# Kernel tuning notes

Hardware: AMD Instinct MI355X
Metric: run time of the kernel (lower is better)

The kernel has to match this reference:

```python
import jax, jax.numpy as jnp
import numpy as np

B, S, D, H, FF = 8, 1024, 2048, 16, 8192
Dh = D // H
EPS = 1e-5

def _layernorm(x, g, b):
    m = jnp.mean(x, axis=-1, keepdims=True)
    v = jnp.mean(jnp.square(x - m), axis=-1, keepdims=True)
    return (x - m) / jnp.sqrt(v + EPS) * g + b

def setup_inputs() -> dict:
    key = jax.random.key(0)
    ks = jax.random.split(key, 12)
    sc_d = 1.0 / np.sqrt(D)
    sc_ff = 1.0 / np.sqrt(FF)
    return {
        "x": jax.random.normal(ks[0], (B, S, D), dtype=jnp.float32),
        "mask": jnp.ones((S, S), dtype=jnp.int32),
        "Wq": jax.random.normal(ks[1], (D, D), dtype=jnp.float32) * sc_d,
        "bq": jnp.zeros((D,), dtype=jnp.float32),
        "Wk": jax.random.normal(ks[2], (D, D), dtype=jnp.float32) * sc_d,
        "bk": jnp.zeros((D,), dtype=jnp.float32),
        "Wv": jax.random.normal(ks[3], (D, D), dtype=jnp.float32) * sc_d,
        "bv": jnp.zeros((D,), dtype=jnp.float32),
        "Wo": jax.random.normal(ks[4], (D, D), dtype=jnp.float32) * sc_d,
        "bo": jnp.zeros((D,), dtype=jnp.float32),
        "W1": jax.random.normal(ks[5], (FF, D), dtype=jnp.float32) * sc_d,
        "b1": jnp.zeros((FF,), dtype=jnp.float32),
        "W2": jax.random.normal(ks[6], (D, FF), dtype=jnp.float32) * sc_ff,
        "b2": jnp.zeros((D,), dtype=jnp.float32),
        "g1": jnp.ones((D,), dtype=jnp.float32),
        "be1": jnp.zeros((D,), dtype=jnp.float32),
        "g2": jnp.ones((D,), dtype=jnp.float32),
        "be2": jnp.zeros((D,), dtype=jnp.float32),
    }

def reference(x, mask, Wq, bq, Wk, bk, Wv, bv, Wo, bo, W1, b1, W2, b2, g1, be1, g2, be2):
    # --- multi-head attention (chunk along d_model == reshape to heads) ---
    q = (x @ Wq.T + bq).reshape(B, S, H, Dh)
    k = (x @ Wk.T + bk).reshape(B, S, H, Dh)
    v = (x @ Wv.T + bv).reshape(B, S, H, Dh)
    score = jnp.einsum('bqhd,bkhd->bhqk', q, k) / jnp.sqrt(jnp.float32(Dh))
    score = jnp.where(mask == 0, jnp.float32(-1e9), score)
    attn = jax.nn.softmax(score, axis=-1)
    out = jnp.einsum('bhqk,bkhd->bqhd', attn, v).reshape(B, S, D)
    attn_out = out @ Wo.T + bo
    # --- residual + post-LN ---
    x1 = _layernorm(attn_out + x, g1, be1)
    # --- FFN ---
    h = jax.nn.relu(x1 @ W1.T + b1)
    ffn_out = h @ W2.T + b2
    return _layernorm(ffn_out + x1, g2, be2)
```

## Files before the change

kernel.cpp:

```cpp
#include <hip/hip_runtime.h>
#include <cstdint>
#include <cstddef>


typedef unsigned short u16;
typedef unsigned int   u32;
typedef unsigned long long u64;
typedef __attribute__((ext_vector_type(8))) short short8;
typedef __attribute__((ext_vector_type(4))) float f32x4;

constexpr int Bc  = 8;
constexpr int Sc  = 1024;
constexpr int Dc  = 2048;
constexpr int Hc  = 16;
constexpr int Dhc = 128;
constexpr int FFc = 8192;
constexpr int Mc  = Bc * Sc;

__device__ __forceinline__ u16 f2b(float f) {
  u32 u = __builtin_bit_cast(u32, f);
  u += 0x7fffu + ((u >> 16) & 1u);
  return (u16)(u >> 16);
}
__device__ __forceinline__ u32 pack2(float a, float b) {
  return (u32)f2b(a) | ((u32)f2b(b) << 16);
}
__device__ __forceinline__ void unpack8(uint4 u, float* f) {
  u32 w[4] = {u.x, u.y, u.z, u.w};
#pragma unroll
  for (int i = 0; i < 4; ++i) {
    f[2 * i + 0] = __builtin_bit_cast(float, w[i] << 16);
    f[2 * i + 1] = __builtin_bit_cast(float, w[i] & 0xffff0000u);
  }
}

#define GLOAD_LDS16(gp, lp)                                                    \
  __builtin_amdgcn_global_load_lds(                                            \
      (const __attribute__((address_space(1))) void*)(gp),                     \
      (__attribute__((address_space(3))) void*)(lp), 16, 0, 0)

__global__ __launch_bounds__(256) void cvt_f32_bf16(const float* __restrict__ in,
                                                    u16* __restrict__ out, int n) {
  int i = (blockIdx.x * 256 + threadIdx.x) << 2;
  if (i >= n) return;
  float4 v = *(const float4*)(in + i);
  ushort4 o;
  o.x = f2b(v.x); o.y = f2b(v.y); o.z = f2b(v.z); o.w = f2b(v.w);
  *(ushort4*)(out + i) = o;
}

__global__ __launch_bounds__(256) void cvt4(const float* __restrict__ s0, u16* __restrict__ d0,
                                            const float* __restrict__ s1, u16* __restrict__ d1,
                                            const float* __restrict__ s2, u16* __restrict__ d2,
                                            const float* __restrict__ s3, u16* __restrict__ d3) {
  int b = blockIdx.x;
  const float* src; u16* dst; int rb;
  if (b < 16384)      { src = s0; dst = d0; rb = b; }
  else if (b < 20480) { src = s1; dst = d1; rb = b - 16384; }
  else if (b < 24576) { src = s2; dst = d2; rb = b - 20480; }
  else                { src = s3; dst = d3; rb = b - 24576; }
  int i = (rb * 256 + (int)threadIdx.x) << 2;
  float4 v = *(const float4*)(src + i);
  ushort4 o;
  o.x = f2b(v.x); o.y = f2b(v.y); o.z = f2b(v.z); o.w = f2b(v.w);
  *(ushort4*)(dst + i) = o;
}

__global__ __launch_bounds__(256) void mask_bits(const int* __restrict__ mask,
                                                 u64* __restrict__ mb) {
  int t = blockIdx.x * 256 + threadIdx.x;
  int r = t >> 4, wd = t & 15;
  const int* p = mask + (size_t)r * Sc + wd * 64;
  u64 bits = 0;
#pragma unroll 16
  for (int i = 0; i < 64; i += 4) {
    int4 q = *(const int4*)(p + i);
    bits |= (u64)(q.x != 0) << (i + 0);
    bits |= (u64)(q.y != 0) << (i + 1);
    bits |= (u64)(q.z != 0) << (i + 2);
    bits |= (u64)(q.w != 0) << (i + 3);
  }
  mb[t] = bits;
}

template <int MODE>
__global__ __launch_bounds__(512, 2) void gemm256tb(const u16* __restrict__ A,
                                                    const u16* __restrict__ Bt,
                                                    const float* __restrict__ bias,
                                                    const float* __restrict__ bias2,
                                                    const float* __restrict__ bias3,
                                                    u16* __restrict__ C,
                                                    int M, int N, int K) {
  __shared__ u16 Abuf[4][256 * 32];
  __shared__ u16 Bbuf[4][256 * 32];

  const int nbn = N >> 8;
  const int nwg = (M >> 8) * nbn;
  int bid = blockIdx.x;
  int sw = (bid & 7) * (nwg >> 3) + (bid >> 3);
  const int m0 = (sw / nbn) << 8;
  const int n0 = (sw % nbn) << 8;

  const int tid  = threadIdx.x;
  const int lane = tid & 63;
  const int w    = tid >> 6;
  const int wm   = w >> 2;
  const int wn   = w & 3;

  const int rowA = lane & 15;
  const int g4   = lane >> 4;

  const int p16  = lane << 4;
  const int wsw  = p16 ^ (((p16 >> 9) & 1) << 5);
  const int s_rr = wsw >> 6;
  const int s_cc = (wsw & 63) >> 1;

  const int sb = (rowA * 64 + g4 * 16) ^ (((rowA >> 3) & 1) << 5);

  const int NT = K >> 5;

  const u16* aP = A  + (size_t)(m0 + w * 32 + s_rr) * K + s_cc;
  const u16* bP = Bt + (size_t)(n0 + w * 32 + s_rr) * K + s_cc;
  const size_t rstep = (size_t)16 * K;

  auto stage = [&](int tt, const u16* ap, const u16* bp) {
    int buf = tt & 3;
    GLOAD_LDS16(ap,         &Abuf[buf][(2 * w + 0) * 512]);
    GLOAD_LDS16(ap + rstep, &Abuf[buf][(2 * w + 1) * 512]);
    GLOAD_LDS16(bp,         &Bbuf[buf][(2 * w + 0) * 512]);
    GLOAD_LDS16(bp + rstep, &Bbuf[buf][(2 * w + 1) * 512]);
  };

  auto readF = [&](int tt, short8* aF, short8* bF) {
    int buf = tt & 3;
#pragma unroll
    for (int n = 0; n < 4; ++n)
      bF[n] = *(const short8*)((const char*)&Bbuf[buf][(wn * 4 + n) * 512] + sb);
#pragma unroll
    for (int i = 0; i < 8; ++i)
      aF[i] = *(const short8*)((const char*)&Abuf[buf][(wm * 8 + i) * 512] + sb);
  };

  f32x4 acc[8][4];
#pragma unroll
  for (int m = 0; m < 8; ++m)
#pragma unroll
    for (int n = 0; n < 4; ++n) acc[m][n] = (f32x4){0.f, 0.f, 0.f, 0.f};

  stage(0, aP, bP);
  stage(1, aP + 32, bP + 32);
  stage(2, aP + 64, bP + 64);
  aP += 96; bP += 96;
  asm volatile("s_waitcnt vmcnt(4)" ::: "memory");
  __builtin_amdgcn_s_barrier();

  short8 a0[8], b0[4], a1[8], b1[4];
  readF(0, a0, b0);

  auto body = [&](int t, short8* aC, short8* bC, short8* aN, short8* bN) {
    if (t + 1 < NT) readF(t + 1, aN, bN);
    if (t + 3 < NT) { stage(t + 3, aP, bP); aP += 32; bP += 32; }
#pragma unroll
    for (int i = 0; i < 8; ++i)
#pragma unroll
      for (int n = 0; n < 4; ++n)
        acc[i][n] = __builtin_amdgcn_mfma_f32_16x16x32_bf16(aC[i], bC[n], acc[i][n], 0, 0, 0);
    if (t + 3 < NT) { asm volatile("s_waitcnt vmcnt(4)" ::: "memory"); }
    else            { asm volatile("s_waitcnt vmcnt(0)" ::: "memory"); }
    __builtin_amdgcn_s_barrier();
  };

  for (int t = 0; t < NT; t += 2) {
    body(t,     a0, b0, a1, b1);
    body(t + 1, a1, b1, a0, b0);
  }

  const int ci = lane & 15;
  const int ri = g4 << 2;

  if (MODE == 3) {
    const int cb   = n0 + wn * 64;
    const int seg  = cb >> 11;
    const int cseg = cb & 2047;
    const float* bp_ = (seg == 0) ? bias : (seg == 1) ? bias2 : bias3;
    float bvv[4];
#pragma unroll
    for (int n = 0; n < 4; ++n) bvv[n] = bp_[cseg + n * 16 + ci];
    if (seg < 2) {
      u16* Cs = C + (size_t)seg * Mc * Dc;
#pragma unroll
      for (int m = 0; m < 8; ++m) {
        int row0 = m0 + wm * 128 + m * 16 + ri;
#pragma unroll
        for (int j = 0; j < 4; ++j) {
          u16* cp = Cs + (size_t)(row0 + j) * Dc + cseg + ci;
#pragma unroll
          for (int n = 0; n < 4; ++n)
            cp[n * 16] = f2b(acc[m][n][j] + bvv[n]);
        }
      }
    } else {
      u16* Cv = C + (size_t)2 * Mc * Dc;
#pragma unroll
      for (int n = 0; n < 4; ++n) {
        int col = cseg + n * 16 + ci;
#pragma unroll
        for (int m = 0; m < 8; ++m) {
          int row0 = m0 + wm * 128 + m * 16 + ri;
          ushort4 pk;
          pk.x = f2b(acc[m][n][0] + bvv[n]);
          pk.y = f2b(acc[m][n][1] + bvv[n]);
          pk.z = f2b(acc[m][n][2] + bvv[n]);
          pk.w = f2b(acc[m][n][3] + bvv[n]);
          size_t addr = ((size_t)((row0 >> 10) * Hc + (col >> 7)) * 128 + (col & 127)) * 1024
                        + (row0 & 1023);
          *(ushort4*)(Cv + addr) = pk;
        }
      }
    }
  } else {
    float bvv[4];
#pragma unroll
    for (int n = 0; n < 4; ++n) bvv[n] = bias[n0 + wn * 64 + n * 16 + ci];
#pragma unroll
    for (int m = 0; m < 8; ++m) {
      int row0 = m0 + wm * 128 + m * 16 + ri;
#pragma unroll
      for (int j = 0; j < 4; ++j) {
        u16* cp = C + (size_t)(row0 + j) * N + n0 + wn * 64 + ci;
#pragma unroll
        for (int n = 0; n < 4; ++n) {
          float v = acc[m][n][j] + bvv[n];
          if (MODE == 1) v = fmaxf(v, 0.f);
          cp[n * 16] = f2b(v);
        }
      }
    }
  }
}

__global__ __launch_bounds__(256, 2) void attn_mfma(
    const u16* __restrict__ qb,
    const u16* __restrict__ kb,
    const u16* __restrict__ vt,
    const u64* __restrict__ mb,
    u16* __restrict__ ob)
{
  __shared__ u16 Ks[64 * 128];
  __shared__ u16 Vts[128 * 64];
  __shared__ u16 Ps[4][32 * 64];

  const int bid = blockIdx.x;
  const int l   = (bid & 7) * 128 + (bid >> 3);
  const int qt  = l & 7;
  const int bh  = l >> 3;
  const int h   = bh & (Hc - 1);
  const int b   = bh >> 4;
  const int q0  = qt * 128;

  const int tid  = threadIdx.x;
  const int lane = tid & 63;
  const int w    = tid >> 6;
  const int rowA = lane & 15;
  const int g4   = lane >> 4;
  const int kq16 = g4 << 3;
  const int ri   = g4 << 2;

  const size_t tokbase = (size_t)b * Sc * Dc + (size_t)h * Dhc;
  const size_t vtbase  = (size_t)bh * 128 * 1024;
  const int qwbase = q0 + w * 32;

  short8 qf[2][4];
#pragma unroll
  for (int m = 0; m < 2; ++m)
#pragma unroll
    for (int kk = 0; kk < 4; ++kk)
      qf[m][kk] = *reinterpret_cast<const short8*>(
          qb + tokbase + (size_t)(qwbase + m * 16 + rowA) * Dc + kk * 32 + kq16);

  f32x4 O[2][8];
#pragma unroll
  for (int m = 0; m < 2; ++m)
#pragma unroll
    for (int n = 0; n < 8; ++n) O[m][n] = (f32x4){0.f, 0.f, 0.f, 0.f};
  float mrow[2][4], lrow[2][4];
#pragma unroll
  for (int m = 0; m < 2; ++m)
#pragma unroll
    for (int j = 0; j < 4; ++j) { mrow[m][j] = -INFINITY; lrow[m][j] = 0.f; }

  const float scale = 0.08838834764831845f;

  for (int kt = 0; kt < Sc / 64; ++kt) {
    const int k0 = kt * 64;
    __syncthreads();
#pragma unroll
    for (int i = 0; i < 4; ++i) {
      int chunk = w * 4 + i;
      int gb = (chunk * 64 + lane) * 16;
      int L  = gb ^ (((gb >> 8) & 7) << 4);
      int row = L >> 8, ce = (L & 255) >> 1;
      GLOAD_LDS16(kb + tokbase + (size_t)(k0 + row) * Dc + ce, &Ks[chunk * 512]);
    }
#pragma unroll
    for (int i = 0; i < 4; ++i) {
      int chunk = w * 4 + i;
      int gb = (chunk * 64 + lane) * 16;
      int L  = gb ^ (((gb >> 7) & 7) << 4);
      int row = L >> 7, ce = (L & 127) >> 1;
      GLOAD_LDS16(vt + vtbase + (size_t)row * 1024 + k0 + ce, &Vts[chunk * 512]);
    }
    __syncthreads();

    f32x4 s[2][4];
#pragma unroll
    for (int m = 0; m < 2; ++m)
#pragma unroll
      for (int n = 0; n < 4; ++n) s[m][n] = (f32x4){0.f, 0.f, 0.f, 0.f};
#pragma unroll
    for (int kk = 0; kk < 4; ++kk) {
      short8 bfk[4];
#pragma unroll
      for (int n = 0; n < 4; ++n) {
        int krow = n * 16 + rowA;
        int by = (krow * 256 + kk * 64 + (g4 << 4)) ^ ((krow & 7) << 4);
        bfk[n] = *reinterpret_cast<const short8*>((const char*)Ks + by);
      }
#pragma unroll
      for (int m = 0; m < 2; ++m)
#pragma unroll
        for (int n = 0; n < 4; ++n)
          s[m][n] = __builtin_amdgcn_mfma_f32_16x16x32_bf16(qf[m][kk], bfk[n], s[m][n], 0, 0, 0);
    }

    float mx[2][4];
#pragma unroll
    for (int m = 0; m < 2; ++m) {
      u64 wb_[4];
#pragma unroll
      for (int j = 0; j < 4; ++j)
        wb_[j] = mb[(size_t)(qwbase + m * 16 + ri + j) * 16 + kt];
#pragma unroll
      for (int j = 0; j < 4; ++j) {
        float mj = -3.0e38f;
#pragma unroll
        for (int n = 0; n < 4; ++n) {
          float x = s[m][n][j] * scale;
          if (!((wb_[j] >> (n * 16 + rowA)) & 1)) x = -1e9f;
          s[m][n][j] = x;
          mj = fmaxf(mj, x);
        }
        mj = fmaxf(mj, __shfl_xor(mj, 1));
        mj = fmaxf(mj, __shfl_xor(mj, 2));
        mj = fmaxf(mj, __shfl_xor(mj, 4));
        mj = fmaxf(mj, __shfl_xor(mj, 8));
        mx[m][j] = mj;
      }
    }

    float worst = -3.0e38f;
#pragma unroll
    for (int m = 0; m < 2; ++m)
#pragma unroll
      for (int j = 0; j < 4; ++j) worst = fmaxf(worst, mx[m][j] - mrow[m][j]);
    if (__any(worst > 8.f)) {
      float alpha[2][4];
#pragma unroll
      for (int m = 0; m < 2; ++m)
#pragma unroll
        for (int j = 0; j < 4; ++j) {
          float mnew = fmaxf(mrow[m][j], mx[m][j]);
          alpha[m][j] = __expf(mrow[m][j] - mnew);
          mrow[m][j] = mnew;
          lrow[m][j] *= alpha[m][j];
        }
#pragma unroll
      for (int m = 0; m < 2; ++m)
#pragma unroll
        for (int n = 0; n < 8; ++n)
#pragma unroll
          for (int j = 0; j < 4; ++j) O[m][n][j] *= alpha[m][j];
    }

#pragma unroll
    for (int m = 0; m < 2; ++m)
#pragma unroll
      for (int j = 0; j < 4; ++j) {
        float rs_ = 0.f;
        int prow = m * 16 + ri + j;
#pragma unroll
        for (int n = 0; n < 4; ++n) {
          float p = __expf(s[m][n][j] - mrow[m][j]);
          rs_ += p;
          int by = (prow * 128 + 2 * (n * 16 + rowA)) ^ ((prow & 7) << 4);
          *(u16*)((char*)Ps[w] + by) = f2b(p);
        }
        rs_ += __shfl_xor(rs_, 1);
        rs_ += __shfl_xor(rs_, 2);
        rs_ += __shfl_xor(rs_, 4);
        rs_ += __shfl_xor(rs_, 8);
        lrow[m][j] += rs_;
      }
    asm volatile("s_waitcnt lgkmcnt(0)" ::: "memory");

    short8 pa[2][2];
#pragma unroll
    for (int m = 0; m < 2; ++m)
#pragma unroll
      for (int kk = 0; kk < 2; ++kk) {
        int prow = m * 16 + rowA;
        int by = (prow * 128 + kk * 64 + (g4 << 4)) ^ ((prow & 7) << 4);
        pa[m][kk] = *reinterpret_cast<const short8*>((const char*)Ps[w] + by);
      }
#pragma unroll
    for (int kk = 0; kk < 2; ++kk)
#pragma unroll
      for (int n = 0; n < 8; ++n) {
        int drow = n * 16 + rowA;
        int by = (drow * 128 + kk * 64 + (g4 << 4)) ^ ((drow & 7) << 4);
        short8 bfv = *reinterpret_cast<const short8*>((const char*)Vts + by);
#pragma unroll
        for (int m = 0; m < 2; ++m)
          O[m][n] = __builtin_amdgcn_mfma_f32_16x16x32_bf16(pa[m][kk], bfv, O[m][n], 0, 0, 0);
      }
  }

  float inv[2][4];
#pragma unroll
  for (int m = 0; m < 2; ++m)
#pragma unroll
    for (int j = 0; j < 4; ++j) inv[m][j] = 1.f / lrow[m][j];
#pragma unroll
  for (int m = 0; m < 2; ++m)
#pragma unroll
    for (int n = 0; n < 8; ++n) {
      int dcol = n * 16 + rowA;
#pragma unroll
      for (int j = 0; j < 4; ++j) {
        int qg = qwbase + m * 16 + ri + j;
        ob[tokbase + (size_t)qg * Dc + dcol] = f2b(O[m][n][j] * inv[m][j]);
      }
    }
}

template <int RES_BF16, int OUT_BF16>
__global__ __launch_bounds__(256) void ln_kernel(const u16* __restrict__ a,
                                                 const void* __restrict__ resid,
                                                 const float* __restrict__ g,
                                                 const float* __restrict__ be,
                                                 void* __restrict__ out) {
  int row = blockIdx.x;
  int tid = threadIdx.x;
  int c0  = tid << 3;

  float v[8], vr[8];
  uint4 ua = *(const uint4*)(a + (size_t)row * Dc + c0);
  unpack8(ua, v);
  if (RES_BF16) {
    uint4 ur = *(const uint4*)((const u16*)resid + (size_t)row * Dc + c0);
    unpack8(ur, vr);
  } else {
    const float* rp = (const float*)resid + (size_t)row * Dc + c0;
    float4 f0 = *(const float4*)rp;
    float4 f1 = *(const float4*)(rp + 4);
    vr[0] = f0.x; vr[1] = f0.y; vr[2] = f0.z; vr[3] = f0.w;
    vr[4] = f1.x; vr[5] = f1.y; vr[6] = f1.z; vr[7] = f1.w;
  }

  float s = 0.f, ss = 0.f;
#pragma unroll
  for (int j = 0; j < 8; ++j) {
    v[j] += vr[j];
    s += v[j];
    ss += v[j] * v[j];
  }
#pragma unroll
  for (int off = 32; off; off >>= 1) {
    s  += __shfl_down(s, off);
    ss += __shfl_down(ss, off);
  }
  __shared__ float rs[4], rss[4], stat[2];
  if ((tid & 63) == 0) { rs[tid >> 6] = s; rss[tid >> 6] = ss; }
  __syncthreads();
  if (tid == 0) {
    float t  = rs[0] + rs[1] + rs[2] + rs[3];
    float tt = rss[0] + rss[1] + rss[2] + rss[3];
    float mean = t * (1.f / Dc);
    float var  = tt * (1.f / Dc) - mean * mean;
    stat[0] = mean;
    stat[1] = rsqrtf(var + 1e-5f);
  }
  __syncthreads();
  float mean = stat[0], rstd = stat[1];

  float y[8];
#pragma unroll
  for (int j = 0; j < 8; ++j) y[j] = (v[j] - mean) * rstd * g[c0 + j] + be[c0 + j];

  if (OUT_BF16) {
    uint4 o;
    o.x = pack2(y[0], y[1]); o.y = pack2(y[2], y[3]);
    o.z = pack2(y[4], y[5]); o.w = pack2(y[6], y[7]);
    *(uint4*)((u16*)out + (size_t)row * Dc + c0) = o;
  } else {
    float* op = (float*)out + (size_t)row * Dc + c0;
    *(float4*)op       = (float4){y[0], y[1], y[2], y[3]};
    *(float4*)(op + 4) = (float4){y[4], y[5], y[6], y[7]};
  }
}

extern "C" void kernel_launch(void* const* d_in, const int* in_sizes, int n_in,
                              void* d_out, int out_size, void* d_ws, size_t ws_size,
                              hipStream_t stream) {
  (void)in_sizes; (void)n_in; (void)out_size; (void)ws_size;

  const float* x   = (const float*)d_in[0];
  const int*   mk  = (const int*)d_in[1];
  const float* Wq  = (const float*)d_in[2];
  const float* bq  = (const float*)d_in[3];
  const float* Wk  = (const float*)d_in[4];
  const float* bk  = (const float*)d_in[5];
  const float* Wv  = (const float*)d_in[6];
  const float* bv  = (const float*)d_in[7];
  const float* Wo  = (const float*)d_in[8];
  const float* bo  = (const float*)d_in[9];
  const float* W1  = (const float*)d_in[10];
  const float* b1  = (const float*)d_in[11];
  const float* W2  = (const float*)d_in[12];
  const float* b2  = (const float*)d_in[13];
  const float* g1  = (const float*)d_in[14];
  const float* be1 = (const float*)d_in[15];
  const float* g2  = (const float*)d_in[16];
  const float* be2 = (const float*)d_in[17];
  float* outp = (float*)d_out;

  const size_t R = 16777216;
  u16* xb   = (u16*)d_ws;
  u16* wqkv = xb + R;
  u64* mbt  = (u64*)(wqkv + 13 * 1024 * 1024);
  u16* qb   = xb + 2 * R;
  u16* ao   = xb + 5 * R;
  u16* wst6 = xb + 6 * R;
  u16* x1   = xb + 6 * R;
  u16* ap   = xb + 7 * R;
  u16* w1s  = xb;
  u16* hb   = xb + 2 * R;
  u16* w2s  = xb + 7 * R;
  u16* ffn  = wqkv;

  const size_t MD = (size_t)Mc * Dc;

  auto cvt = [&](const float* src, u16* dst, int n) {
    cvt_f32_bf16<<<dim3((n + 1023) / 1024), dim3(256), 0, stream>>>(src, dst, n);
  };

  cvt4<<<dim3(28672), dim3(256), 0, stream>>>(x, xb,
                                              Wq, wqkv,
                                              Wk, wqkv + Dc * Dc,
                                              Wv, wqkv + 2 * Dc * Dc);

  gemm256tb<3><<<dim3(32 * 24), dim3(512), 0, stream>>>(xb, wqkv, bq, bk, bv,
                                                        qb, Mc, 3 * Dc, Dc);

  mask_bits<<<dim3(64), dim3(256), 0, stream>>>(mk, mbt);

  attn_mfma<<<dim3(Bc * Hc * (Sc / 128)), dim3(256), 0, stream>>>(
      qb, qb + MD, qb + 2 * MD, mbt, ao);

  cvt(Wo, wst6, Dc * Dc);
  gemm256tb<0><<<dim3(32 * 8), dim3(512), 0, stream>>>(ao, wst6, bo, bo, bo,
                                                       ap, Mc, Dc, Dc);
  ln_kernel<0, 1><<<dim3(Mc), dim3(256), 0, stream>>>(ap, x, g1, be1, x1);

  cvt(W1, w1s, FFc * Dc);
  gemm256tb<1><<<dim3(32 * 32), dim3(512), 0, stream>>>(x1, w1s, b1, b1, b1,
                                                        hb, Mc, FFc, Dc);
  cvt(W2, w2s, Dc * FFc);
  gemm256tb<0><<<dim3(32 * 8), dim3(512), 0, stream>>>(hb, w2s, b2, b2, b2,
                                                       ffn, Mc, Dc, FFc);
  ln_kernel<1, 0><<<dim3(Mc), dim3(256), 0, stream>>>(ffn, x1, g2, be2, outp);
}
```

Baseline: 1.058 ms.

## Switch GEMM inner loop from 16x16x32 to 32x32x16 bf16 MFMA tiles

Replaces the 8x4 grid of 16x16x32 MFMA accumulators per wave with a 4x2 grid of 32x32x16 MFMA accumulators, issuing two k-steps per 32-wide k tile. LDS fragment reads and the epilogue index mapping are rewritten for the 32x32 output layout. The aim is fewer MFMA instructions and fewer LDS fragment loads per tile, since the larger instruction reuses each operand across more output. The risk is that the new swizzled LDS offsets or epilogue mapping cause bank conflicts or less coalesced stores.

```diff
diff --git a/kernel.cpp b/kernel.cpp
--- a/kernel.cpp
+++ b/kernel.cpp
@@ -6,8 +6,9 @@
 typedef unsigned short u16;
 typedef unsigned int   u32;
 typedef unsigned long long u64;
-typedef __attribute__((ext_vector_type(8))) short short8;
-typedef __attribute__((ext_vector_type(4))) float f32x4;
+typedef __attribute__((ext_vector_type(8)))  short short8;
+typedef __attribute__((ext_vector_type(4)))  float f32x4;
+typedef __attribute__((ext_vector_type(16))) float f32x16;
 
 constexpr int Bc  = 8;
 constexpr int Sc  = 1024;
@@ -107,15 +108,19 @@
   const int wm   = w >> 2;
   const int wn   = w & 3;
 
-  const int rowA = lane & 15;
-  const int g4   = lane >> 4;
-
   const int p16  = lane << 4;
   const int wsw  = p16 ^ (((p16 >> 9) & 1) << 5);
   const int s_rr = wsw >> 6;
   const int s_cc = (wsw & 63) >> 1;
 
-  const int sb = (rowA * 64 + g4 * 16) ^ (((rowA >> 3) & 1) << 5);
+  const int rl    = lane & 31;
+  const int kh    = lane >> 5;
+  const int r16   = rl & 15;
+  const int sub32 = rl >> 4;
+  const int xv    = ((r16 >> 3) & 1) << 5;
+  const int sA    = sub32 * 1024 + r16 * 64;
+  const int k0o   = (kh * 16) ^ xv;
+  const int k1o   = (32 + kh * 16) ^ xv;
 
   const int NT = K >> 5;
 
@@ -131,21 +136,27 @@
     GLOAD_LDS16(bp + rstep, &Bbuf[buf][(2 * w + 1) * 512]);
   };
 
-  auto readF = [&](int tt, short8* aF, short8* bF) {
+  auto readF = [&](int tt, short8 aF[4][2], short8 bF[2][2]) {
     int buf = tt & 3;
-#pragma unroll
-    for (int n = 0; n < 4; ++n)
-      bF[n] = *(const short8*)((const char*)&Bbuf[buf][(wn * 4 + n) * 512] + sb);
-#pragma unroll
-    for (int i = 0; i < 8; ++i)
-      aF[i] = *(const short8*)((const char*)&Abuf[buf][(wm * 8 + i) * 512] + sb);
+    const char* ab = (const char*)&Abuf[buf][0] + wm * 8192 + sA;
+    const char* bb = (const char*)&Bbuf[buf][0] + wn * 4096 + sA;
+#pragma unroll
+    for (int n = 0; n < 2; ++n) {
+      bF[n][0] = *(const short8*)(bb + n * 2048 + k0o);
+      bF[n][1] = *(const short8*)(bb + n * 2048 + k1o);
+    }
+#pragma unroll
+    for (int i = 0; i < 4; ++i) {
+      aF[i][0] = *(const short8*)(ab + i * 2048 + k0o);
+      aF[i][1] = *(const short8*)(ab + i * 2048 + k1o);
+    }
   };
 
-  f32x4 acc[8][4];
-#pragma unroll
-  for (int m = 0; m < 8; ++m)
-#pragma unroll
-    for (int n = 0; n < 4; ++n) acc[m][n] = (f32x4){0.f, 0.f, 0.f, 0.f};
+  f32x16 acc[4][2];
+#pragma unroll
+  for (int i = 0; i < 4; ++i)
+#pragma unroll
+    for (int n = 0; n < 2; ++n) acc[i][n] = (f32x16)(0.f);
 
   stage(0, aP, bP);
   stage(1, aP + 32, bP + 32);
@@ -154,17 +165,21 @@
   asm volatile("s_waitcnt vmcnt(4)" ::: "memory");
   __builtin_amdgcn_s_barrier();
 
-  short8 a0[8], b0[4], a1[8], b1[4];
+  short8 a0[4][2], b0[2][2], a1[4][2], b1[2][2];
   readF(0, a0, b0);
 
-  auto body = [&](int t, short8* aC, short8* bC, short8* aN, short8* bN) {
+  auto body = [&](int t, short8 aC[4][2], short8 bC[2][2],
+                  short8 aN[4][2], short8 bN[2][2]) {
     if (t + 1 < NT) readF(t + 1, aN, bN);
     if (t + 3 < NT) { stage(t + 3, aP, bP); aP += 32; bP += 32; }
 #pragma unroll
-    for (int i = 0; i < 8; ++i)
-#pragma unroll
-      for (int n = 0; n < 4; ++n)
-        acc[i][n] = __builtin_amdgcn_mfma_f32_16x16x32_bf16(aC[i], bC[n], acc[i][n], 0, 0, 0);
+    for (int ks = 0; ks < 2; ++ks)
+#pragma unroll
+      for (int i = 0; i < 4; ++i)
+#pragma unroll
+        for (int n = 0; n < 2; ++n)
+          acc[i][n] = __builtin_amdgcn_mfma_f32_32x32x16_bf16(aC[i][ks], bC[n][ks],
+                                                              acc[i][n], 0, 0, 0);
     if (t + 3 < NT) { asm volatile("s_waitcnt vmcnt(4)" ::: "memory"); }
     else            { asm volatile("s_waitcnt vmcnt(0)" ::: "memory"); }
     __builtin_amdgcn_s_barrier();
@@ -174,67 +189,74 @@
     body(t,     a0, b0, a1, b1);
     body(t + 1, a1, b1, a0, b0);
   }
-
-  const int ci = lane & 15;
-  const int ri = g4 << 2;
 
   if (MODE == 3) {
     const int cb   = n0 + wn * 64;
     const int seg  = cb >> 11;
     const int cseg = cb & 2047;
     const float* bp_ = (seg == 0) ? bias : (seg == 1) ? bias2 : bias3;
-    float bvv[4];
-#pragma unroll
-    for (int n = 0; n < 4; ++n) bvv[n] = bp_[cseg + n * 16 + ci];
+    float bvv[2];
+#pragma unroll
+    for (int n = 0; n < 2; ++n) bvv[n] = bp_[cseg + n * 32 + rl];
     if (seg < 2) {
       u16* Cs = C + (size_t)seg * Mc * Dc;
 #pragma unroll
-      for (int m = 0; m < 8; ++m) {
-        int row0 = m0 + wm * 128 + m * 16 + ri;
-#pragma unroll
-        for (int j = 0; j < 4; ++j) {
-          u16* cp = Cs + (size_t)(row0 + j) * Dc + cseg + ci;
-#pragma unroll
-          for (int n = 0; n < 4; ++n)
-            cp[n * 16] = f2b(acc[m][n][j] + bvv[n]);
-        }
+      for (int i = 0; i < 4; ++i) {
+        int rowb = m0 + wm * 128 + i * 32 + kh * 4;
+#pragma unroll
+        for (int q = 0; q < 4; ++q)
+#pragma unroll
+          for (int r = 0; r < 4; ++r) {
+            int row = rowb + q * 8 + r;
+            u16* cp = Cs + (size_t)row * Dc + cseg + rl;
+#pragma unroll
+            for (int n = 0; n < 2; ++n)
+              cp[n * 32] = f2b(acc[i][n][q * 4 + r] + bvv[n]);
+          }
       }
     } else {
       u16* Cv = C + (size_t)2 * Mc * Dc;
 #pragma unroll
-      for (int n = 0; n < 4; ++n) {
-        int col = cseg + n * 16 + ci;
-#pragma unroll
-        for (int m = 0; m < 8; ++m) {
-          int row0 = m0 + wm * 128 + m * 16 + ri;
-          ushort4 pk;
-          pk.x = f2b(acc[m][n][0] + bvv[n]);
-          pk.y = f2b(acc[m][n][1] + bvv[n]);
-          pk.z = f2b(acc[m][n][2] + bvv[n]);
-          pk.w = f2b(acc[m][n][3] + bvv[n]);
-          size_t addr = ((size_t)((row0 >> 10) * Hc + (col >> 7)) * 128 + (col & 127)) * 1024
-                        + (row0 & 1023);
-          *(ushort4*)(Cv + addr) = pk;
+      for (int n = 0; n < 2; ++n) {
+        int colv = cseg + n * 32 + rl;
+#pragma unroll
+        for (int i = 0; i < 4; ++i) {
+          int rowb = m0 + wm * 128 + i * 32 + kh * 4;
+#pragma unroll
+          for (int q = 0; q < 4; ++q) {
+            int row0 = rowb + q * 8;
+            ushort4 pk;
+            pk.x = f2b(acc[i][n][q * 4 + 0] + bvv[n]);
+            pk.y = f2b(acc[i][n][q * 4 + 1] + bvv[n]);
+            pk.z = f2b(acc[i][n][q * 4 + 2] + bvv[n]);
+            pk.w = f2b(acc[i][n][q * 4 + 3] + bvv[n]);
+            size_t addr = ((size_t)((row0 >> 10) * Hc + (colv >> 7)) * 128 + (colv & 127)) * 1024
+                          + (row0 & 1023);
+            *(ushort4*)(Cv + addr) = pk;
+          }
         }
       }
     }
   } else {
-    float bvv[4];
-#pragma unroll
-    for (int n = 0; n < 4; ++n) bvv[n] = bias[n0 + wn * 64 + n * 16 + ci];
-#pragma unroll
-    for (int m = 0; m < 8; ++m) {
-      int row0 = m0 + wm * 128 + m * 16 + ri;
-#pragma unroll
-      for (int j = 0; j < 4; ++j) {
-        u16* cp = C + (size_t)(row0 + j) * N + n0 + wn * 64 + ci;
-#pragma unroll
-        for (int n = 0; n < 4; ++n) {
-          float v = acc[m][n][j] + bvv[n];
-          if (MODE == 1) v = fmaxf(v, 0.f);
-          cp[n * 16] = f2b(v);
+    float bvv[2];
+#pragma unroll
+    for (int n = 0; n < 2; ++n) bvv[n] = bias[n0 + wn * 64 + n * 32 + rl];
+#pragma unroll
+    for (int i = 0; i < 4; ++i) {
+      int rowb = m0 + wm * 128 + i * 32 + kh * 4;
+#pragma unroll
+      for (int q = 0; q < 4; ++q)
+#pragma unroll
+        for (int r = 0; r < 4; ++r) {
+          int row = rowb + q * 8 + r;
+          u16* cp = C + (size_t)row * N + n0 + wn * 64 + rl;
+#pragma unroll
+          for (int n = 0; n < 2; ++n) {
+            float v = acc[i][n][q * 4 + r] + bvv[n];
+            if (MODE == 1) v = fmaxf(v, 0.f);
+            cp[n * 32] = f2b(v);
+          }
         }
-      }
     }
   }
 }
```

After: 1.125 ms. 6.4% more time.

## Split GEMM main loop into two half-phases with interleaved loads and MFMA priority

Applied to the files above, without the earlier changes.

Restructures the bf16 GEMM inner loop. The whole-tile LDS fragment prefetch into double-buffered registers is replaced by two phases per k-step: read half of the A fragments plus the B fragments, issue the A global-to-LDS stage, compute; then read the other A half, issue the B stage, compute. It adds s_setprio around the MFMA blocks and extra barriers so waves interleave memory and matrix work. The aim is to cut register pressure and spread global loads across the step, at the cost of more barriers and losing the register-level prefetch of the next tile.

```diff
diff --git a/kernel.cpp b/kernel.cpp
--- a/kernel.cpp
+++ b/kernel.cpp
@@ -123,56 +123,68 @@
   const u16* bP = Bt + (size_t)(n0 + w * 32 + s_rr) * K + s_cc;
   const size_t rstep = (size_t)16 * K;
 
-  auto stage = [&](int tt, const u16* ap, const u16* bp) {
+  auto stageA = [&](int tt, const u16* ap) {
     int buf = tt & 3;
     GLOAD_LDS16(ap,         &Abuf[buf][(2 * w + 0) * 512]);
     GLOAD_LDS16(ap + rstep, &Abuf[buf][(2 * w + 1) * 512]);
+  };
+  auto stageB = [&](int tt, const u16* bp) {
+    int buf = tt & 3;
     GLOAD_LDS16(bp,         &Bbuf[buf][(2 * w + 0) * 512]);
     GLOAD_LDS16(bp + rstep, &Bbuf[buf][(2 * w + 1) * 512]);
   };
 
-  auto readF = [&](int tt, short8* aF, short8* bF) {
-    int buf = tt & 3;
-#pragma unroll
-    for (int n = 0; n < 4; ++n)
-      bF[n] = *(const short8*)((const char*)&Bbuf[buf][(wn * 4 + n) * 512] + sb);
-#pragma unroll
-    for (int i = 0; i < 8; ++i)
-      aF[i] = *(const short8*)((const char*)&Abuf[buf][(wm * 8 + i) * 512] + sb);
-  };
-
   f32x4 acc[8][4];
 #pragma unroll
   for (int m = 0; m < 8; ++m)
 #pragma unroll
     for (int n = 0; n < 4; ++n) acc[m][n] = (f32x4){0.f, 0.f, 0.f, 0.f};
 
-  stage(0, aP, bP);
-  stage(1, aP + 32, bP + 32);
-  stage(2, aP + 64, bP + 64);
+  stageA(0, aP); stageB(0, bP);
+  stageA(1, aP + 32); stageB(1, bP + 32);
+  stageA(2, aP + 64); stageB(2, bP + 64);
   aP += 96; bP += 96;
   asm volatile("s_waitcnt vmcnt(4)" ::: "memory");
   __builtin_amdgcn_s_barrier();
 
-  short8 a0[8], b0[4], a1[8], b1[4];
-  readF(0, a0, b0);
-
-  auto body = [&](int t, short8* aC, short8* bC, short8* aN, short8* bN) {
-    if (t + 1 < NT) readF(t + 1, aN, bN);
-    if (t + 3 < NT) { stage(t + 3, aP, bP); aP += 32; bP += 32; }
-#pragma unroll
-    for (int i = 0; i < 8; ++i)
+  for (int t = 0; t < NT; ++t) {
+    const int buf = t & 3;
+    const bool st = (t + 3) < NT;
+
+    short8 bF[4], aF[4];
+#pragma unroll
+    for (int n = 0; n < 4; ++n)
+      bF[n] = *(const short8*)((const char*)&Bbuf[buf][(wn * 4 + n) * 512] + sb);
+#pragma unroll
+    for (int i = 0; i < 4; ++i)
+      aF[i] = *(const short8*)((const char*)&Abuf[buf][(wm * 8 + i) * 512] + sb);
+    if (st) stageA(t + 3, aP);
+    __builtin_amdgcn_s_barrier();
+    __builtin_amdgcn_s_setprio(1);
+#pragma unroll
+    for (int i = 0; i < 4; ++i)
 #pragma unroll
       for (int n = 0; n < 4; ++n)
-        acc[i][n] = __builtin_amdgcn_mfma_f32_16x16x32_bf16(aC[i], bC[n], acc[i][n], 0, 0, 0);
-    if (t + 3 < NT) { asm volatile("s_waitcnt vmcnt(4)" ::: "memory"); }
-    else            { asm volatile("s_waitcnt vmcnt(0)" ::: "memory"); }
+        acc[i][n] = __builtin_amdgcn_mfma_f32_16x16x32_bf16(aF[i], bF[n], acc[i][n], 0, 0, 0);
+    __builtin_amdgcn_s_setprio(0);
     __builtin_amdgcn_s_barrier();
-  };
-
-  for (int t = 0; t < NT; t += 2) {
-    body(t,     a0, b0, a1, b1);
-    body(t + 1, a1, b1, a0, b0);
+
+    short8 aG[4];
+#pragma unroll
+    for (int i = 0; i < 4; ++i)
+      aG[i] = *(const short8*)((const char*)&Abuf[buf][(wm * 8 + 4 + i) * 512] + sb);
+    if (st) { stageB(t + 3, bP); aP += 32; bP += 32; }
+    __builtin_amdgcn_s_barrier();
+    __builtin_amdgcn_s_setprio(1);
+#pragma unroll
+    for (int i = 0; i < 4; ++i)
+#pragma unroll
+      for (int n = 0; n < 4; ++n)
+        acc[4 + i][n] = __builtin_amdgcn_mfma_f32_16x16x32_bf16(aG[i], bF[n], acc[4 + i][n], 0, 0, 0);
+    __builtin_amdgcn_s_setprio(0);
+    if (st) { asm volatile("s_waitcnt vmcnt(4)" ::: "memory"); }
+    else    { asm volatile("s_waitcnt vmcnt(0)" ::: "memory"); }
+    __builtin_amdgcn_s_barrier();
   }
 
   const int ci = lane & 15;
```

Result: slower. 1.151 ms (+8.8%).
